# Optimization experiments

Hardware: AMD Instinct MI355X
Metric: run time of the kernel (lower is better)

The kernel has to match this reference:

```python
import jax, jax.numpy as jnp
import numpy as np

D_MODEL = 1024
NUM_HEADS = 16
THETA = 10000.0
B, T = 2, 2048


def _rope(x, pos, theta_base):
    # x: (b, h, t, d_h); interleaved pairs (x0,x1),(x2,x3),... per the
    # rearrange '... (c d) -> ... c d' with d=2 in the original module.
    d = x.shape[-1]
    half = d // 2
    inv_freq = 1.0 / (theta_base ** (2.0 * jnp.arange(half, dtype=jnp.float32) / d))
    ang = pos.astype(jnp.float32)[:, None] * inv_freq[None, :]  # (t, half)
    sin = jnp.sin(ang)[None, None]  # (1,1,t,half)
    cos = jnp.cos(ang)[None, None]
    x1 = x[..., 0::2]
    x2 = x[..., 1::2]
    r1 = x1 * cos - x2 * sin
    r2 = x1 * sin + x2 * cos
    return jnp.stack([r1, r2], axis=-1).reshape(x.shape)


def setup_inputs() -> dict:
    key = jax.random.key(0)
    k0, k1, k2, k3, k4 = jax.random.split(key, 5)
    sigma = (2.0 / (D_MODEL + D_MODEL)) ** 0.5
    return {
        "in_features": jax.random.normal(k0, (B, T, D_MODEL), dtype=jnp.float32),
        "Wq": jax.random.normal(k1, (D_MODEL, D_MODEL), dtype=jnp.float32) * sigma,
        "Wk": jax.random.normal(k2, (D_MODEL, D_MODEL), dtype=jnp.float32) * sigma,
        "Wv": jax.random.normal(k3, (D_MODEL, D_MODEL), dtype=jnp.float32) * sigma,
        "Wo": jax.random.normal(k4, (D_MODEL, D_MODEL), dtype=jnp.float32) * sigma,
        "token_positions": jnp.arange(T, dtype=jnp.int32),
    }


def reference(in_features, Wq, Wk, Wv, Wo, token_positions):
    b, t, d_model = in_features.shape
    h = NUM_HEADS
    d_h = d_model // h
    # Fused-style QKV projections (x @ W.T, weights stored (in, out))
    q = in_features @ Wq.T
    k = in_features @ Wk.T
    v = in_features @ Wv.T
    # (b, t, h*d_h) -> (b, h, t, d_h)
    q = q.reshape(b, t, h, d_h).transpose(0, 2, 1, 3)
    k = k.reshape(b, t, h, d_h).transpose(0, 2, 1, 3)
    v = v.reshape(b, t, h, d_h).transpose(0, 2, 1, 3)
    q = _rope(q, token_positions, THETA)
    k = _rope(k, token_positions, THETA)
    scale = 1.0 / jnp.sqrt(jnp.asarray(d_h, dtype=q.dtype))
    scores = jnp.einsum('bhqd,bhkd->bhqk', q, k) * scale
    causal = jnp.tril(jnp.ones((t, t), dtype=bool))
    scores = jnp.where(causal[None, None], scores, -jnp.inf)
    attn = jax.nn.softmax(scores, axis=-1)
    out = jnp.einsum('bhqk,bhkd->bhqd', attn, v)
    out = out.transpose(0, 2, 1, 3).reshape(b, t, h * d_h)
    return out @ Wo.T
```

## Files before the change

kernel.cpp:

```cpp
#include <hip/hip_runtime.h>

#define D_MODEL 1024
#define NUM_HEADS 16
#define DH 64
#define B_SZ 2
#define T_SZ 2048
#define M_ROWS (B_SZ * T_SZ)

typedef __bf16 bf16;
typedef __bf16 bf16x4 __attribute__((ext_vector_type(4)));
typedef __bf16 bf16x8 __attribute__((ext_vector_type(8)));
typedef float f32x4 __attribute__((ext_vector_type(4)));

__device__ __forceinline__ void async_copy16(const bf16* g, bf16* l) {
  __builtin_amdgcn_global_load_lds(
      (const __attribute__((address_space(1))) void*)g,
      (__attribute__((address_space(3))) void*)l, 16, 0, 0);
}

#define NX (M_ROWS * D_MODEL / 4)
#define NW (D_MODEL * D_MODEL / 4)

__global__ __launch_bounds__(256) void cast_all(
    const float* __restrict__ X, const float* __restrict__ Wq,
    const float* __restrict__ Wk, const float* __restrict__ Wv,
    const float* __restrict__ Wo,
    bf16* __restrict__ Xb, bf16* __restrict__ Wqb, bf16* __restrict__ Wkb,
    bf16* __restrict__ Wvb, bf16* __restrict__ Wob) {
  int i = blockIdx.x * 256 + threadIdx.x;
  const float* s; bf16* d; int off;
  if (i < NX) {
    s = X; d = Xb; off = i;
  } else {
    int j = i - NX;
    int w = j >> 18;
    off = j & (NW - 1);
    if (w == 0)      { s = Wq; d = Wqb; }
    else if (w == 1) { s = Wk; d = Wkb; }
    else if (w == 2) { s = Wv; d = Wvb; }
    else             { s = Wo; d = Wob; }
  }
  float4 v = ((const float4*)s)[off];
  bf16x4 o;
  o[0] = (bf16)v.x; o[1] = (bf16)v.y; o[2] = (bf16)v.z; o[3] = (bf16)v.w;
  ((bf16x4*)d)[off] = o;
}

#define KLN 0.28782313662425f
#define BK 32
#define NKT (D_MODEL / BK)

__global__ __launch_bounds__(512, 2) void qkv_gemm(
    const bf16* __restrict__ Xb,
    const bf16* __restrict__ Wqb, const bf16* __restrict__ Wkb,
    const bf16* __restrict__ Wvb, const int* __restrict__ pos,
    bf16* __restrict__ Q, bf16* __restrict__ K, bf16* __restrict__ VT) {
  __shared__ bf16 LA[4][256 * BK];
  __shared__ bf16 LB[4][256 * BK];

  int tid = threadIdx.x;
  int wave = tid >> 6, lane = tid & 63;
  int wm = wave >> 2, wn = wave & 3;
  int l15 = lane & 15, quad = lane >> 4;

  int row0 = blockIdx.x * 256;
  int col0 = blockIdx.y * 256;
  int sel = col0 >> 10;
  int nb = col0 & 1023;
  const bf16* W = (sel == 0) ? Wqb : (sel == 1) ? Wkb : Wvb;

  int srow = tid >> 2;
  int scol = 8 * ((tid & 3) ^ ((tid >> 3) & 3));
  const bf16* Ag = Xb + (size_t)(row0 + srow) * D_MODEL + scol;
  const bf16* Bg = W + (size_t)(nb + srow) * D_MODEL + scol;
  int ldst = tid * 8;

  int swz = 8 * (quad ^ ((l15 >> 1) & 3));
  int aoff = (wm * 128 + l15) * BK + swz;
  int boff = (wn * 64 + l15) * BK + swz;

  f32x4 acc[8][4];
#pragma unroll
  for (int mi = 0; mi < 8; ++mi)
#pragma unroll
    for (int nj = 0; nj < 4; ++nj) acc[mi][nj] = (f32x4){0.f, 0.f, 0.f, 0.f};

#pragma unroll
  for (int pt = 0; pt < 3; ++pt) {
    int k0 = pt * BK;
    async_copy16(Ag + k0, &LA[pt][ldst]);
    async_copy16(Ag + k0 + (size_t)128 * D_MODEL, &LA[pt][ldst + 4096]);
    async_copy16(Bg + k0, &LB[pt][ldst]);
    async_copy16(Bg + k0 + (size_t)128 * D_MODEL, &LB[pt][ldst + 4096]);
  }
  asm volatile("s_waitcnt vmcnt(8)" ::: "memory");
  __builtin_amdgcn_s_barrier();
  __builtin_amdgcn_sched_barrier(0);

  for (int kt = 0; kt < NKT; ++kt) {
    const bf16* La = LA[kt & 3];
    const bf16* Lb = LB[kt & 3];
    bf16x8 a[8], b[4];
#pragma unroll
    for (int mi = 0; mi < 8; ++mi)
      a[mi] = *(const bf16x8*)&La[aoff + mi * 16 * BK];
#pragma unroll
    for (int nj = 0; nj < 4; ++nj)
      b[nj] = *(const bf16x8*)&Lb[boff + nj * 16 * BK];

    if (kt < NKT - 3) {
      int k0 = (kt + 3) * BK;
      int bq = (kt + 3) & 3;
      async_copy16(Ag + k0, &LA[bq][ldst]);
      async_copy16(Ag + k0 + (size_t)128 * D_MODEL, &LA[bq][ldst + 4096]);
      async_copy16(Bg + k0, &LB[bq][ldst]);
      async_copy16(Bg + k0 + (size_t)128 * D_MODEL, &LB[bq][ldst + 4096]);
      asm volatile("s_waitcnt vmcnt(8) lgkmcnt(0)" ::: "memory");
    } else {
      asm volatile("s_waitcnt vmcnt(0) lgkmcnt(0)" ::: "memory");
    }
    __builtin_amdgcn_s_barrier();
    __builtin_amdgcn_sched_barrier(0);

    __builtin_amdgcn_s_setprio(1);
#pragma unroll
    for (int mi = 0; mi < 8; ++mi)
#pragma unroll
      for (int nj = 0; nj < 4; ++nj)
        acc[mi][nj] = __builtin_amdgcn_mfma_f32_16x16x32_bf16(
            a[mi], b[nj], acc[mi][nj], 0, 0, 0);
    __builtin_amdgcn_s_setprio(0);
  }

  if (sel == 1) {
    bool even = (l15 & 1) == 0;
#pragma unroll
    for (int nj = 0; nj < 4; ++nj) {
      float fr = __expf(-(float)((nj * 16 + (l15 & 14)) >> 1) * KLN);
#pragma unroll
      for (int mi = 0; mi < 8; ++mi)
#pragma unroll
        for (int r = 0; r < 4; ++r) {
          float p = (float)pos[(row0 + wm * 128 + mi * 16 + quad * 4 + r) &
                               (T_SZ - 1)];
          float v = acc[mi][nj][r];
          float pn = __shfl_xor(v, 1);
          float s, c;
          __sincosf(p * fr, &s, &c);
          acc[mi][nj][r] = even ? (v * c - pn * s) : (pn * s + v * c);
        }
    }
  }

  if (sel == 2) {
    int b = row0 >> 11;
    int t0 = row0 & (T_SZ - 1);
#pragma unroll
    for (int mi = 0; mi < 8; ++mi) {
      int t = t0 + wm * 128 + mi * 16 + quad * 4;
#pragma unroll
      for (int nj = 0; nj < 4; ++nj) {
        int col = nb + wn * 64 + nj * 16 + l15;
        int h = col >> 6;
        int d = col & 63;
        bf16x4 ov;
#pragma unroll
        for (int r = 0; r < 4; ++r) ov[r] = (bf16)acc[mi][nj][r];
        *(bf16x4*)&VT[((size_t)(b * NUM_HEADS + h) * DH + d) * T_SZ + t] = ov;
      }
    }
  } else {
    bf16* Out = (sel == 0) ? Q : K;
#pragma unroll
    for (int mi = 0; mi < 8; ++mi) {
      int row = row0 + wm * 128 + mi * 16 + quad * 4;
#pragma unroll
      for (int nj = 0; nj < 4; ++nj) {
        int col = nb + wn * 64 + nj * 16 + l15;
#pragma unroll
        for (int r = 0; r < 4; ++r)
          Out[(size_t)(row + r) * D_MODEL + col] = (bf16)acc[mi][nj][r];
      }
    }
  }
}

#define PST 72
#define KST 72

__global__ __launch_bounds__(256) void attn_kernel(
    const bf16* __restrict__ Q, const bf16* __restrict__ K,
    const bf16* __restrict__ VT, const int* __restrict__ pos,
    bf16* __restrict__ AO) {
  __shared__ bf16 Kt[64 * KST];
  __shared__ bf16 Vt[64 * KST];
  __shared__ bf16 Pbuf[4][16 * PST];

  int bh = blockIdx.x;
  int qi = 31 - (int)blockIdx.y;
  int bb = bh >> 4, h = bh & 15;
  int tid = threadIdx.x;
  int wave = tid >> 6, lane = tid & 63;
  int l15 = lane & 15, quad = lane >> 4;

  int q0 = qi * 64 + wave * 16;
  size_t grow = (size_t)bb * T_SZ + q0;

  const bf16* Qp = Q + (grow + l15) * D_MODEL + h * DH + quad * 8;
  bf16x8 bq0 = *(const bf16x8*)(Qp);
  bf16x8 bq1 = *(const bf16x8*)(Qp + 32);
  {
    float p = (float)pos[q0 + l15];
#pragma unroll
    for (int jj = 0; jj < 4; ++jj) {
      int i0 = quad * 4 + jj;
      float s, c;
      __sincosf(p * __expf(-(float)i0 * KLN), &s, &c);
      float x1 = (float)bq0[2 * jj], x2 = (float)bq0[2 * jj + 1];
      bq0[2 * jj]     = (bf16)(x1 * c - x2 * s);
      bq0[2 * jj + 1] = (bf16)(x1 * s + x2 * c);
      __sincosf(p * __expf(-(float)(i0 + 16) * KLN), &s, &c);
      float y1 = (float)bq1[2 * jj], y2 = (float)bq1[2 * jj + 1];
      bq1[2 * jj]     = (bf16)(y1 * c - y2 * s);
      bq1[2 * jj + 1] = (bf16)(y1 * s + y2 * c);
    }
  }

  f32x4 o[4];
#pragma unroll
  for (int nt = 0; nt < 4; ++nt) o[nt] = (f32x4){0.f, 0.f, 0.f, 0.f};
  float l_i = 0.f;

  int srow = tid >> 2;
  int sc = (tid & 3) * 16;
  const bf16* Kg = K + ((size_t)bb * T_SZ + srow) * D_MODEL + h * DH + sc;
  const bf16* Vg = VT + ((size_t)bh * DH + srow) * T_SZ + sc;
  bf16* Kl = &Kt[srow * KST + sc];
  bf16* Vl = &Vt[srow * KST + sc];

  bf16* Pw = Pbuf[wave];
  int nchunks = qi + 1;
  int rel = wave * 16 + l15;

  bf16x8 kr0 = *(const bf16x8*)(Kg);
  bf16x8 kr1 = *(const bf16x8*)(Kg + 8);
  bf16x8 vr0 = *(const bf16x8*)(Vg);
  bf16x8 vr1 = *(const bf16x8*)(Vg + 8);

  for (int t = 0; t < nchunks; ++t) {
    __syncthreads();
    *(bf16x8*)(Kl) = kr0;
    *(bf16x8*)(Kl + 8) = kr1;
    *(bf16x8*)(Vl) = vr0;
    *(bf16x8*)(Vl + 8) = vr1;
    if (t + 1 < nchunks) {
      const bf16* Kn = Kg + (size_t)(t + 1) * 64 * D_MODEL;
      const bf16* Vn = Vg + (t + 1) * 64;
      kr0 = *(const bf16x8*)(Kn);
      kr1 = *(const bf16x8*)(Kn + 8);
      vr0 = *(const bf16x8*)(Vn);
      vr1 = *(const bf16x8*)(Vn + 8);
    }
    __syncthreads();

    f32x4 st[4];
#pragma unroll
    for (int cs = 0; cs < 4; ++cs) {
      bf16x8 ak0 = *(const bf16x8*)&Kt[(cs * 16 + l15) * KST + quad * 8];
      bf16x8 ak1 = *(const bf16x8*)&Kt[(cs * 16 + l15) * KST + 32 + quad * 8];
      f32x4 s4 = (f32x4){0.f, 0.f, 0.f, 0.f};
      s4 = __builtin_amdgcn_mfma_f32_16x16x32_bf16(ak0, bq0, s4, 0, 0, 0);
      s4 = __builtin_amdgcn_mfma_f32_16x16x32_bf16(ak1, bq1, s4, 0, 0, 0);
      st[cs] = s4;
    }

    bool last = (t == nchunks - 1);
    float ps = 0.f;
#pragma unroll
    for (int cs = 0; cs < 4; ++cs)
#pragma unroll
      for (int r = 0; r < 4; ++r) {
        float p = __expf(st[cs][r] * 0.125f);
        if (last) {
          int cl = cs * 16 + quad * 4 + r;
          p = (cl > rel) ? 0.f : p;
        }
        st[cs][r] = p;
        ps += p;
      }
    l_i += ps;

#pragma unroll
    for (int cs = 0; cs < 4; ++cs) {
      bf16x4 pk;
#pragma unroll
      for (int r = 0; r < 4; ++r) pk[r] = (bf16)st[cs][r];
      *(bf16x4*)&Pw[l15 * PST + cs * 16 + quad * 4] = pk;
    }
    __asm__ __volatile__("" ::: "memory");
    bf16x8 bp0 = *(const bf16x8*)&Pw[l15 * PST + quad * 8];
    bf16x8 bp1 = *(const bf16x8*)&Pw[l15 * PST + 32 + quad * 8];
    __asm__ __volatile__("" ::: "memory");

#pragma unroll
    for (int nt = 0; nt < 4; ++nt) {
      bf16x8 av0 = *(const bf16x8*)&Vt[(nt * 16 + l15) * KST + quad * 8];
      bf16x8 av1 = *(const bf16x8*)&Vt[(nt * 16 + l15) * KST + 32 + quad * 8];
      o[nt] = __builtin_amdgcn_mfma_f32_16x16x32_bf16(av0, bp0, o[nt], 0, 0, 0);
      o[nt] = __builtin_amdgcn_mfma_f32_16x16x32_bf16(av1, bp1, o[nt], 0, 0, 0);
    }
  }

  l_i += __shfl_xor(l_i, 16);
  l_i += __shfl_xor(l_i, 32);
  float inv = 1.0f / l_i;
#pragma unroll
  for (int nt = 0; nt < 4; ++nt) {
    bf16x4 ov;
#pragma unroll
    for (int r = 0; r < 4; ++r) ov[r] = (bf16)(o[nt][r] * inv);
    *(bf16x4*)&AO[(grow + l15) * D_MODEL + h * DH + nt * 16 + quad * 4] = ov;
  }
}

__global__ __launch_bounds__(256) void out_gemm(
    const bf16* __restrict__ AO, const bf16* __restrict__ Wob,
    float* __restrict__ out) {
  __shared__ bf16 As[128 * 32];
  __shared__ bf16 Bs[64 * 32];

  int tid = threadIdx.x;
  int wave = tid >> 6, lane = tid & 63;
  int l15 = lane & 15, quad = lane >> 4;

  int row0 = blockIdx.x * 128;
  int nb = blockIdx.y * 64;

  int srow = tid >> 2;
  int schunk = tid & 3;
  const bf16* Ag = AO + (size_t)(row0 + srow) * D_MODEL + schunk * 8;
  const bf16* Bg = Wob + (size_t)(nb + srow) * D_MODEL + schunk * 8;
  bf16* Al0 = &As[srow * 32 + schunk * 8];
  bf16* Al1 = &As[(srow + 64) * 32 + schunk * 8];
  bf16* Bl = &Bs[srow * 32 + schunk * 8];

  f32x4 acc[2][4];
#pragma unroll
  for (int i = 0; i < 2; ++i)
#pragma unroll
    for (int j = 0; j < 4; ++j) acc[i][j] = (f32x4){0.f, 0.f, 0.f, 0.f};

  for (int k0 = 0; k0 < D_MODEL; k0 += 32) {
    async_copy16(Ag + k0, Al0);
    async_copy16(Ag + k0 + (size_t)64 * D_MODEL, Al1);
    async_copy16(Bg + k0, Bl);
    __syncthreads();

    bf16x8 af[2], bfr[4];
#pragma unroll
    for (int i = 0; i < 2; ++i)
      af[i] = *(const bf16x8*)&As[(wave * 32 + i * 16 + l15) * 32 + quad * 8];
#pragma unroll
    for (int j = 0; j < 4; ++j)
      bfr[j] = *(const bf16x8*)&Bs[(j * 16 + l15) * 32 + quad * 8];
#pragma unroll
    for (int i = 0; i < 2; ++i)
#pragma unroll
      for (int j = 0; j < 4; ++j)
        acc[i][j] = __builtin_amdgcn_mfma_f32_16x16x32_bf16(af[i], bfr[j],
                                                            acc[i][j], 0, 0, 0);
    __syncthreads();
  }

#pragma unroll
  for (int i = 0; i < 2; ++i) {
    int row = row0 + wave * 32 + i * 16 + quad * 4;
#pragma unroll
    for (int j = 0; j < 4; ++j) {
      int col = nb + j * 16 + l15;
#pragma unroll
      for (int r = 0; r < 4; ++r)
        out[(size_t)(row + r) * D_MODEL + col] = acc[i][j][r];
    }
  }
}

extern "C" void kernel_launch(void* const* d_in, const int* in_sizes, int n_in,
                              void* d_out, int out_size, void* d_ws, size_t ws_size,
                              hipStream_t stream) {
  const float* X  = (const float*)d_in[0];
  const float* Wq = (const float*)d_in[1];
  const float* Wk = (const float*)d_in[2];
  const float* Wv = (const float*)d_in[3];
  const float* Wo = (const float*)d_in[4];
  const int*  pos = (const int*)d_in[5];
  float* out = (float*)d_out;

  char* w = (char*)d_ws;
  bf16* Xb  = (bf16*)w;  w += (size_t)M_ROWS * D_MODEL * 2;
  bf16* Wqb = (bf16*)w;  w += (size_t)D_MODEL * D_MODEL * 2;
  bf16* Wkb = (bf16*)w;  w += (size_t)D_MODEL * D_MODEL * 2;
  bf16* Wvb = (bf16*)w;  w += (size_t)D_MODEL * D_MODEL * 2;
  bf16* Wob = (bf16*)w;  w += (size_t)D_MODEL * D_MODEL * 2;
  bf16* Qb  = (bf16*)w;  w += (size_t)M_ROWS * D_MODEL * 2;
  bf16* Kb  = (bf16*)w;  w += (size_t)M_ROWS * D_MODEL * 2;
  bf16* VT  = (bf16*)w;  w += (size_t)M_ROWS * D_MODEL * 2;
  bf16* AO  = (bf16*)w;  w += (size_t)M_ROWS * D_MODEL * 2;

  cast_all<<<(NX + 4 * NW) / 256, 256, 0, stream>>>(X, Wq, Wk, Wv, Wo,
                                                    Xb, Wqb, Wkb, Wvb, Wob);
  qkv_gemm<<<dim3(M_ROWS / 256, 3 * D_MODEL / 256), 512, 0, stream>>>(
      Xb, Wqb, Wkb, Wvb, pos, Qb, Kb, VT);
  attn_kernel<<<dim3(B_SZ * NUM_HEADS, T_SZ / 64), 256, 0, stream>>>(
      Qb, Kb, VT, pos, AO);
  out_gemm<<<dim3(M_ROWS / 128, D_MODEL / 64), 256, 0, stream>>>(AO, Wob, out);
}
```

Baseline: 174.9 us.

## Shrink QKV GEMM tile to 128x256 with 3-stage pipeline; reorder attention block schedule

The QKV projection GEMM tile goes from 256x256 to 128x256 per block, with a 3-buffer LDS pipeline instead of 4 and launch bounds raised to allow more blocks per CU. This doubles the grid so all CUs get work and cuts LDS and register use per block, at the cost of less reuse of each loaded B tile. Separately, the attention kernel's query-block order changes from strictly reversed to a serpentine order within groups of eight. That alters how heavy and light causal blocks spread over the GPU.

```diff
diff --git a/kernel.cpp b/kernel.cpp
--- a/kernel.cpp
+++ b/kernel.cpp
@@ -50,20 +50,20 @@
 #define BK 32
 #define NKT (D_MODEL / BK)
 
-__global__ __launch_bounds__(512, 2) void qkv_gemm(
+__global__ __launch_bounds__(512, 4) void qkv_gemm(
     const bf16* __restrict__ Xb,
     const bf16* __restrict__ Wqb, const bf16* __restrict__ Wkb,
     const bf16* __restrict__ Wvb, const int* __restrict__ pos,
     bf16* __restrict__ Q, bf16* __restrict__ K, bf16* __restrict__ VT) {
-  __shared__ bf16 LA[4][256 * BK];
-  __shared__ bf16 LB[4][256 * BK];
+  __shared__ bf16 LA[3][128 * BK];
+  __shared__ bf16 LB[3][256 * BK];
 
   int tid = threadIdx.x;
   int wave = tid >> 6, lane = tid & 63;
   int wm = wave >> 2, wn = wave & 3;
   int l15 = lane & 15, quad = lane >> 4;
 
-  int row0 = blockIdx.x * 256;
+  int row0 = blockIdx.x * 128;
   int col0 = blockIdx.y * 256;
   int sel = col0 >> 10;
   int nb = col0 & 1023;
@@ -76,46 +76,45 @@
   int ldst = tid * 8;
 
   int swz = 8 * (quad ^ ((l15 >> 1) & 3));
-  int aoff = (wm * 128 + l15) * BK + swz;
+  int aoff = (wm * 64 + l15) * BK + swz;
   int boff = (wn * 64 + l15) * BK + swz;
 
-  f32x4 acc[8][4];
-#pragma unroll
-  for (int mi = 0; mi < 8; ++mi)
+  f32x4 acc[4][4];
+#pragma unroll
+  for (int mi = 0; mi < 4; ++mi)
 #pragma unroll
     for (int nj = 0; nj < 4; ++nj) acc[mi][nj] = (f32x4){0.f, 0.f, 0.f, 0.f};
 
-#pragma unroll
-  for (int pt = 0; pt < 3; ++pt) {
-    int k0 = pt * BK;
-    async_copy16(Ag + k0, &LA[pt][ldst]);
-    async_copy16(Ag + k0 + (size_t)128 * D_MODEL, &LA[pt][ldst + 4096]);
-    async_copy16(Bg + k0, &LB[pt][ldst]);
-    async_copy16(Bg + k0 + (size_t)128 * D_MODEL, &LB[pt][ldst + 4096]);
-  }
-  asm volatile("s_waitcnt vmcnt(8)" ::: "memory");
+#define STAGE(bq, pt)                                                        \
+  do {                                                                       \
+    int k0_ = (pt) * BK;                                                     \
+    async_copy16(Ag + k0_, &LA[bq][ldst]);                                   \
+    async_copy16(Bg + k0_, &LB[bq][ldst]);                                   \
+    async_copy16(Bg + k0_ + (size_t)128 * D_MODEL, &LB[bq][ldst + 4096]);    \
+  } while (0)
+
+  STAGE(0, 0);
+  STAGE(1, 1);
+  asm volatile("s_waitcnt vmcnt(3)" ::: "memory");
   __builtin_amdgcn_s_barrier();
   __builtin_amdgcn_sched_barrier(0);
 
+  int cur = 0;
   for (int kt = 0; kt < NKT; ++kt) {
-    const bf16* La = LA[kt & 3];
-    const bf16* Lb = LB[kt & 3];
-    bf16x8 a[8], b[4];
-#pragma unroll
-    for (int mi = 0; mi < 8; ++mi)
+    const bf16* La = LA[cur];
+    const bf16* Lb = LB[cur];
+    bf16x8 a[4], b[4];
+#pragma unroll
+    for (int mi = 0; mi < 4; ++mi)
       a[mi] = *(const bf16x8*)&La[aoff + mi * 16 * BK];
 #pragma unroll
     for (int nj = 0; nj < 4; ++nj)
       b[nj] = *(const bf16x8*)&Lb[boff + nj * 16 * BK];
 
-    if (kt < NKT - 3) {
-      int k0 = (kt + 3) * BK;
-      int bq = (kt + 3) & 3;
-      async_copy16(Ag + k0, &LA[bq][ldst]);
-      async_copy16(Ag + k0 + (size_t)128 * D_MODEL, &LA[bq][ldst + 4096]);
-      async_copy16(Bg + k0, &LB[bq][ldst]);
-      async_copy16(Bg + k0 + (size_t)128 * D_MODEL, &LB[bq][ldst + 4096]);
-      asm volatile("s_waitcnt vmcnt(8) lgkmcnt(0)" ::: "memory");
+    if (kt + 2 < NKT) {
+      int nbuf = cur + 2 >= 3 ? cur - 1 : cur + 2;
+      STAGE(nbuf, kt + 2);
+      asm volatile("s_waitcnt vmcnt(3) lgkmcnt(0)" ::: "memory");
     } else {
       asm volatile("s_waitcnt vmcnt(0) lgkmcnt(0)" ::: "memory");
     }
@@ -124,13 +123,16 @@
 
     __builtin_amdgcn_s_setprio(1);
 #pragma unroll
-    for (int mi = 0; mi < 8; ++mi)
+    for (int mi = 0; mi < 4; ++mi)
 #pragma unroll
       for (int nj = 0; nj < 4; ++nj)
         acc[mi][nj] = __builtin_amdgcn_mfma_f32_16x16x32_bf16(
             a[mi], b[nj], acc[mi][nj], 0, 0, 0);
     __builtin_amdgcn_s_setprio(0);
-  }
+
+    cur = cur == 2 ? 0 : cur + 1;
+  }
+#undef STAGE
 
   if (sel == 1) {
     bool even = (l15 & 1) == 0;
@@ -138,10 +140,10 @@
     for (int nj = 0; nj < 4; ++nj) {
       float fr = __expf(-(float)((nj * 16 + (l15 & 14)) >> 1) * KLN);
 #pragma unroll
-      for (int mi = 0; mi < 8; ++mi)
+      for (int mi = 0; mi < 4; ++mi)
 #pragma unroll
         for (int r = 0; r < 4; ++r) {
-          float p = (float)pos[(row0 + wm * 128 + mi * 16 + quad * 4 + r) &
+          float p = (float)pos[(row0 + wm * 64 + mi * 16 + quad * 4 + r) &
                                (T_SZ - 1)];
           float v = acc[mi][nj][r];
           float pn = __shfl_xor(v, 1);
@@ -156,8 +158,8 @@
     int b = row0 >> 11;
     int t0 = row0 & (T_SZ - 1);
 #pragma unroll
-    for (int mi = 0; mi < 8; ++mi) {
-      int t = t0 + wm * 128 + mi * 16 + quad * 4;
+    for (int mi = 0; mi < 4; ++mi) {
+      int t = t0 + wm * 64 + mi * 16 + quad * 4;
 #pragma unroll
       for (int nj = 0; nj < 4; ++nj) {
         int col = nb + wn * 64 + nj * 16 + l15;
@@ -172,8 +174,8 @@
   } else {
     bf16* Out = (sel == 0) ? Q : K;
 #pragma unroll
-    for (int mi = 0; mi < 8; ++mi) {
-      int row = row0 + wm * 128 + mi * 16 + quad * 4;
+    for (int mi = 0; mi < 4; ++mi) {
+      int row = row0 + wm * 64 + mi * 16 + quad * 4;
 #pragma unroll
       for (int nj = 0; nj < 4; ++nj) {
         int col = nb + wn * 64 + nj * 16 + l15;
@@ -197,7 +199,9 @@
   __shared__ bf16 Pbuf[4][16 * PST];
 
   int bh = blockIdx.x;
-  int qi = 31 - (int)blockIdx.y;
+  int y = blockIdx.y;
+  int yq = y >> 3, yr = y & 7;
+  int qi = 8 * yq + ((yq & 1) ? 7 - yr : yr);
   int bb = bh >> 4, h = bh & 15;
   int tid = threadIdx.x;
   int wave = tid >> 6, lane = tid & 63;
@@ -409,7 +413,7 @@
 
   cast_all<<<(NX + 4 * NW) / 256, 256, 0, stream>>>(X, Wq, Wk, Wv, Wo,
                                                     Xb, Wqb, Wkb, Wvb, Wob);
-  qkv_gemm<<<dim3(M_ROWS / 256, 3 * D_MODEL / 256), 512, 0, stream>>>(
+  qkv_gemm<<<dim3(M_ROWS / 128, 3 * D_MODEL / 256), 512, 0, stream>>>(
       Xb, Wqb, Wkb, Wvb, pos, Qb, Kb, VT);
   attn_kernel<<<dim3(B_SZ * NUM_HEADS, T_SZ / 64), 256, 0, stream>>>(
       Qb, Kb, VT, pos, AO);
```

Measured after the change: 174.9 us. Within noise of the previous version (+0.0%).
